# Kernel optimization log

Hardware: AMD Instinct MI355X
Metric: run time of the kernel (lower is better)

## Reference

```python
import jax, jax.numpy as jnp
import numpy as np

N_LAYERS = 512
Z_INI = 0.0
DEL_Z = 0.9 / 512.0
MU = 1.0
BATCH = 131072


def setup_inputs() -> dict:
    key = jax.random.key(0)
    k1, k2, k3, k4 = jax.random.split(key, 4)
    Re_s = 0.1 * jax.random.normal(k1, (BATCH,), dtype=jnp.float32)
    Im_s = 0.1 * jax.random.normal(k2, (BATCH,), dtype=jnp.float32)
    # omega kept away from 0 (appears in a denominator)
    omega = jax.random.uniform(k3, (BATCH,), dtype=jnp.float32, minval=0.5, maxval=1.5)
    PiT = jnp.ones((1,), dtype=jnp.float32)
    # Bs[j] is Linear(1,1,bias=False)(ones) == its scalar weight; keep near 1 for stability
    B = 1.0 + 0.02 * jax.random.normal(k4, (N_LAYERS + 1,), dtype=jnp.float32)
    return {"Re_s": Re_s, "Im_s": Im_s, "omega": omega, "PiT": PiT, "B": B}


def reference(Re_s, Im_s, omega, PiT, B):
    # forward_1: Euler integration, strict sequential dependence -> lax.scan
    zs = Z_INI + DEL_Z * jnp.arange(N_LAYERS, dtype=jnp.float32)
    B1s = B[:-1]  # Bs[j]
    B2s = B[1:]   # Bs[j+1]
    mu2 = MU * MU

    def step(carry, x):
        Re, Im = carry
        b1, b2, z = x
        inv1 = 1.0 / (PiT * (1.0 - z))          # 1/(PiT (1-z))
        inv2 = inv1 / (1.0 - z)                  # 1/(PiT (1-z)^2)
        g = 1.0 - b2 / b1
        # NOTE: torch updates Re first; Im update uses the NEW Re
        Re_n = Re + g * (Re + inv1) + DEL_Z * (
            2.0 * omega * Im * Re + 2.0 * omega * Im * inv1 - inv2
        )
        Im_n = Im + g * Im + DEL_Z * (
            -omega * inv2 / PiT
            - 2.0 * omega * inv1 * Re_n
            + omega * Im * Im
            - omega * Re_n * Re_n
            + omega / (b1 * b1)
            - z * z * mu2 / (b1 * omega)
        )
        return (Re_n, Im_n), None

    (Re_f, Im_f), _ = jax.lax.scan(step, (Re_s, Im_s), (B1s, B2s, zs))
    return (Re_f, Im_f)
```

## Files before the change

kernel.cpp:

```cpp
#include <hip/hip_runtime.h>

#define N_LAYERS 512
#define DEL_Z (0.9f / 512.0f)
#define NGROUP (N_LAYERS / 4)


#define STEP(C0, C1, I1, C3, C4P)                               \
    {                                                           \
        const float t  = Re + (I1);                             \
        const float a  = fmaf((C0), Re, (C1));                  \
        const float m  = dz2om * Im;                            \
        const float Rn = fmaf(m, t, a);                         \
        const float u  = Rn + (I1);                             \
        float s = fmaf(Im, Im, (C3));                           \
        const float q  = (C4P) * niom;                          \
        const float b  = fmaf((C0), Im, q);                     \
        s = fmaf(-u, u, s);                                     \
        Im = fmaf(dzom, s, b);                                  \
        Re = Rn;                                                \
    }

#define GROUP4(A0, A1, A2, A3, A4)                              \
    STEP((A0).x, (A1).x, (A2).x, (A3).x, (A4).x)                \
    STEP((A0).y, (A1).y, (A2).y, (A3).y, (A4).y)                \
    STEP((A0).z, (A1).z, (A2).z, (A3).z, (A4).z)                \
    STEP((A0).w, (A1).w, (A2).w, (A3).w, (A4).w)

#define LOADG(A0, A1, A2, A3, A4, G)                            \
    {                                                           \
        const float4* cp = cg[(G)];                             \
        (A0) = cp[0]; (A1) = cp[1]; (A2) = cp[2];               \
        (A3) = cp[3]; (A4) = cp[4];                             \
    }

__global__ __launch_bounds__(256) void metric_scan_kernel(
    const float* __restrict__ Re_s, const float* __restrict__ Im_s,
    const float* __restrict__ omega, const float* __restrict__ PiT_p,
    const float* __restrict__ B, float* __restrict__ out, int n)
{
    __shared__ float4 cg[NGROUP][5];

    const float PiT = PiT_p[0];
    float* cbase = (float*)cg;
    for (int l = threadIdx.x; l < N_LAYERS; l += 256) {
        const float z    = DEL_Z * (float)l;
        const float b1   = B[l];
        const float b2   = B[l + 1];
        const float omz  = 1.0f - z;
        const float inv1 = 1.0f / (PiT * omz);
        const float inv2 = inv1 / omz;
        const float g    = 1.0f - b2 / b1;
        float* p = cbase + (l >> 2) * 20 + (l & 3);
        p[0]  = 1.0f + g;
        p[4]  = g * inv1 - DEL_Z * inv2;
        p[8]  = inv1;
        p[12] = inv1 * inv1 - inv2 / PiT + 1.0f / (b1 * b1);
        p[16] = DEL_Z * z * z / b1;
    }
    __syncthreads();

    const int i = blockIdx.x * 256 + threadIdx.x;
    float Re = Re_s[i];
    float Im = Im_s[i];
    const float om    = omega[i];
    const float dzom  = DEL_Z * om;
    const float dz2om = 2.0f * dzom;
    const float niom  = -1.0f / om;

    float4 Pa0, Pa1, Pa2, Pa3, Pa4;
    float4 Pb0, Pb1, Pb2, Pb3, Pb4;
    LOADG(Pa0, Pa1, Pa2, Pa3, Pa4, 0);

    for (int g = 0; g < NGROUP; g += 2) {
        LOADG(Pb0, Pb1, Pb2, Pb3, Pb4, g + 1);
        GROUP4(Pa0, Pa1, Pa2, Pa3, Pa4);
        const int gn = (g + 2 < NGROUP) ? g + 2 : NGROUP - 1;
        LOADG(Pa0, Pa1, Pa2, Pa3, Pa4, gn);
        GROUP4(Pb0, Pb1, Pb2, Pb3, Pb4);
    }

    out[i]     = Re;
    out[n + i] = Im;
}

extern "C" void kernel_launch(void* const* d_in, const int* in_sizes, int n_in,
                              void* d_out, int out_size, void* d_ws, size_t ws_size,
                              hipStream_t stream)
{
    const float* Re_s  = (const float*)d_in[0];
    const float* Im_s  = (const float*)d_in[1];
    const float* omega = (const float*)d_in[2];
    const float* PiT   = (const float*)d_in[3];
    const float* B     = (const float*)d_in[4];
    float* out = (float*)d_out;
    const int n = in_sizes[0];
    metric_scan_kernel<<<n / 256, 256, 0, stream>>>(Re_s, Im_s, omega, PiT, B, out, n);
}
```

Baseline: 22.12 us.

## Reformulate scan in shifted variable t = Re + inv1 and deepen LDS prefetch

The recurrence is rewritten to track t = Re + inv1 instead of Re, folding the per-step inv1 additions into precomputed difference constants, and the per-step omega term is folded into the s accumulation via a per-thread phi factor. This removes roughly one dependent add and one multiply from the serial chain at each of the 512 steps. The shared-memory prefetch is widened to four groups of float4 constants, with the loop unrolled by four groups and kept rolled with pragma unroll 1. The cost is more live registers and some numerical differences from reassociation. The final Re is recovered by subtracting the last inv1, which assumes z ends at 0.9.

Result: slower. 25.06 us (+13.3%).

```diff
diff --git a/kernel.cpp b/kernel.cpp
--- a/kernel.cpp
+++ b/kernel.cpp
@@ -2,22 +2,20 @@
 
 #define N_LAYERS 512
 #define DEL_Z (0.9f / 512.0f)
+#define INV_DEL_Z (512.0f / 0.9f)
 #define NGROUP (N_LAYERS / 4)
 
 
-#define STEP(C0, C1, I1, C3, C4P)                               \
+#define STEP(C0, D1, DL, C3, C4P)                               \
     {                                                           \
-        const float t  = Re + (I1);                             \
-        const float a  = fmaf((C0), Re, (C1));                  \
-        const float m  = dz2om * Im;                            \
-        const float Rn = fmaf(m, t, a);                         \
-        const float u  = Rn + (I1);                             \
+        const float e  = fmaf(dz2om, Im, (C0));                 \
+        const float u  = fmaf(e, t, (D1));                      \
         float s = fmaf(Im, Im, (C3));                           \
-        const float q  = (C4P) * niom;                          \
-        const float b  = fmaf((C0), Im, q);                     \
+        const float bm = (C0) * Im;                             \
         s = fmaf(-u, u, s);                                     \
-        Im = fmaf(dzom, s, b);                                  \
-        Re = Rn;                                                \
+        s = fmaf((C4P), phi, s);                                \
+        Im = fmaf(dzom, s, bm);                                 \
+        t  = u + (DL);                                          \
     }
 
 #define GROUP4(A0, A1, A2, A3, A4)                              \
@@ -43,43 +41,59 @@
     const float PiT = PiT_p[0];
     float* cbase = (float*)cg;
     for (int l = threadIdx.x; l < N_LAYERS; l += 256) {
-        const float z    = DEL_Z * (float)l;
-        const float b1   = B[l];
-        const float b2   = B[l + 1];
-        const float omz  = 1.0f - z;
-        const float inv1 = 1.0f / (PiT * omz);
-        const float inv2 = inv1 / omz;
-        const float g    = 1.0f - b2 / b1;
+        const float z     = DEL_Z * (float)l;
+        const float zn    = DEL_Z * (float)(l + 1);
+        const float b1    = B[l];
+        const float b2    = B[l + 1];
+        const float inv1  = 1.0f / (PiT * (1.0f - z));
+        const float inv1n = 1.0f / (PiT * (1.0f - zn));
+        const float inv2  = inv1 * inv1 * PiT;
         float* p = cbase + (l >> 2) * 20 + (l & 3);
-        p[0]  = 1.0f + g;
-        p[4]  = g * inv1 - DEL_Z * inv2;
-        p[8]  = inv1;
-        p[12] = inv1 * inv1 - inv2 / PiT + 1.0f / (b1 * b1);
+        p[0]  = 2.0f - b2 / b1;
+        p[4]  = -DEL_Z * inv2;
+        p[8]  = inv1n - inv1;
+        p[12] = 1.0f / (b1 * b1);
         p[16] = DEL_Z * z * z / b1;
     }
     __syncthreads();
 
     const int i = blockIdx.x * 256 + threadIdx.x;
-    float Re = Re_s[i];
     float Im = Im_s[i];
     const float om    = omega[i];
     const float dzom  = DEL_Z * om;
     const float dz2om = 2.0f * dzom;
-    const float niom  = -1.0f / om;
+    const float iom   = 1.0f / om;
+    const float phi   = -(iom * iom) * INV_DEL_Z;
+    float t = Re_s[i] + 1.0f / PiT;
 
     float4 Pa0, Pa1, Pa2, Pa3, Pa4;
     float4 Pb0, Pb1, Pb2, Pb3, Pb4;
+    float4 Pc0, Pc1, Pc2, Pc3, Pc4;
+    float4 Pd0, Pd1, Pd2, Pd3, Pd4;
+
     LOADG(Pa0, Pa1, Pa2, Pa3, Pa4, 0);
+    LOADG(Pb0, Pb1, Pb2, Pb3, Pb4, 1);
 
-    for (int g = 0; g < NGROUP; g += 2) {
-        LOADG(Pb0, Pb1, Pb2, Pb3, Pb4, g + 1);
+    #pragma unroll 1
+    for (int it = 0; it < NGROUP / 4; ++it) {
+        const int g  = 4 * it;
+        const int g2 = (g + 2 < NGROUP) ? g + 2 : NGROUP - 1;
+        const int g3 = (g + 3 < NGROUP) ? g + 3 : NGROUP - 1;
+        const int g4 = (g + 4 < NGROUP) ? g + 4 : NGROUP - 1;
+        const int g5 = (g + 5 < NGROUP) ? g + 5 : NGROUP - 1;
+        LOADG(Pc0, Pc1, Pc2, Pc3, Pc4, g2);
         GROUP4(Pa0, Pa1, Pa2, Pa3, Pa4);
-        const int gn = (g + 2 < NGROUP) ? g + 2 : NGROUP - 1;
-        LOADG(Pa0, Pa1, Pa2, Pa3, Pa4, gn);
+        LOADG(Pd0, Pd1, Pd2, Pd3, Pd4, g3);
         GROUP4(Pb0, Pb1, Pb2, Pb3, Pb4);
+        LOADG(Pa0, Pa1, Pa2, Pa3, Pa4, g4);
+        GROUP4(Pc0, Pc1, Pc2, Pc3, Pc4);
+        LOADG(Pb0, Pb1, Pb2, Pb3, Pb4, g5);
+        GROUP4(Pd0, Pd1, Pd2, Pd3, Pd4);
     }
 
-    out[i]     = Re;
+    const float Re_f = t - 1.0f / (PiT * 0.1f);
+
+    out[i]     = Re_f;
     out[n + i] = Im;
 }
 
```
